# Performance work log

Hardware: AMD Instinct MI355X
Metric: run time of the kernel (lower is better)

## Reference

```python
import jax, jax.numpy as jnp
import numpy as np

H = 2048  # hidden_size
B, S = 4, 4096
LEVELS = 3  # hierarchical_compression_levels


def _linear_params(key, out_dim, in_dim):
    kw, kb = jax.random.split(key)
    bound = 1.0 / np.sqrt(in_dim)
    W = jax.random.uniform(kw, (out_dim, in_dim), minval=-bound, maxval=bound, dtype=jnp.float32)
    b = jax.random.uniform(kb, (out_dim,), minval=-bound, maxval=bound, dtype=jnp.float32)
    return W, b


def setup_inputs() -> dict:
    key = jax.random.key(0)
    ks = jax.random.split(key, 12)
    inp = {}
    inp['hidden_states'] = jax.random.normal(ks[0], (B, S, H), dtype=jnp.float32)
    inp['access_frequency'] = jax.random.uniform(ks[1], (B, S), dtype=jnp.float32)
    inp['importance_score'] = jax.random.uniform(ks[2], (B, S), dtype=jnp.float32)
    # compression level 1: H -> H/2 -> H/2 -> H ; level 2: H -> H/4 -> H/4 -> H
    inp['comp1_W'], inp['comp1_b'] = _linear_params(ks[3], H // 2, H)
    inp['adapt1_W'], inp['adapt1_b'] = _linear_params(ks[4], H // 2, H // 2)
    inp['decomp1_W'], inp['decomp1_b'] = _linear_params(ks[5], H, H // 2)
    inp['comp2_W'], inp['comp2_b'] = _linear_params(ks[6], H // 4, H)
    inp['adapt2_W'], inp['adapt2_b'] = _linear_params(ks[7], H // 4, H // 4)
    inp['decomp2_W'], inp['decomp2_b'] = _linear_params(ks[8], H, H // 4)
    # strategy selector: Linear(H, H/4) -> ReLU -> Linear(H/4, LEVELS) -> Softmax
    inp['sel1_W'], inp['sel1_b'] = _linear_params(ks[9], H // 4, H)
    inp['sel2_W'], inp['sel2_b'] = _linear_params(ks[10], LEVELS, H // 4)
    return inp


def reference(hidden_states, access_frequency, importance_score,
              comp1_W, comp1_b, adapt1_W, adapt1_b, decomp1_W, decomp1_b,
              comp2_W, comp2_b, adapt2_W, adapt2_b, decomp2_W, decomp2_b,
              sel1_W, sel1_b, sel2_W, sel2_b):
    h = hidden_states
    h2 = h.shape[-1] // 2
    # _get_compression_strategy: scale first half by freq, second half by importance
    combined = jnp.concatenate(
        [h[..., :h2] * access_frequency[..., None],
         h[..., h2:] * importance_score[..., None]], axis=-1)  # [B,S,H]
    hid = jax.nn.relu(jnp.einsum('bsh,oh->bso', combined, sel1_W) + sel1_b)
    strategy_weights = jax.nn.softmax(jnp.einsum('bso,lo->bsl', hid, sel2_W) + sel2_b, axis=-1)
    selected = jnp.argmax(strategy_weights, axis=-1)  # [B,S] int

    def branch(Wc, bc, Wa, ba, Wd, bd):
        c = jnp.einsum('bsh,oh->bso', h, Wc) + bc          # compress
        c = jnp.einsum('bso,po->bsp', c, Wa) + ba          # frequency adaptor
        return jnp.einsum('bsp,hp->bsh', c, Wd) + bd       # decompress

    out1 = branch(comp1_W, comp1_b, adapt1_W, adapt1_b, decomp1_W, decomp1_b)
    out2 = branch(comp2_W, comp2_b, adapt2_W, adapt2_b, decomp2_W, decomp2_b)
    stacked = jnp.stack([h, out1, out2], axis=2)  # [B,S,LEVELS,H]
    compressed = jnp.take_along_axis(stacked, selected[:, :, None, None], axis=2)[:, :, 0, :]
    return compressed
```

## Files before the change

### kernel.cpp

```cpp
#include <hip/hip_runtime.h>
#include <hip/hip_bf16.h>

#define TOK 16384
#define TAU2 0.001f

typedef __attribute__((ext_vector_type(8))) short short8;
typedef __attribute__((ext_vector_type(4))) float f32x4;

__device__ __forceinline__ unsigned short f32_bf16(float f) {
  __hip_bfloat16 h = __float2bfloat16(f);
  unsigned short u;
  __builtin_memcpy(&u, &h, sizeof(u));
  return u;
}
__device__ __forceinline__ float bf16_f32(unsigned short u) {
  union { unsigned int i; float f; } c; c.i = ((unsigned int)u) << 16; return c.f;
}

__global__ void zero_int(int* p) { if (threadIdx.x == 0) *p = 0; }

__global__ void cvt_kernel(const float* __restrict__ s, unsigned short* __restrict__ d, int n4) {
  int i = blockIdx.x * 256 + threadIdx.x;
  if (i < n4) {
    float4 v = ((const float4*)s)[i];
    union { unsigned short u[4]; uint2 q; } pk;
    pk.u[0] = f32_bf16(v.x); pk.u[1] = f32_bf16(v.y);
    pk.u[2] = f32_bf16(v.z); pk.u[3] = f32_bf16(v.w);
    ((uint2*)d)[i] = pk.q;
  }
}

__global__ void cvt_split_kernel(const float* __restrict__ s,
                                 unsigned short* __restrict__ dhi,
                                 unsigned short* __restrict__ dlo, int n4) {
  int i = blockIdx.x * 256 + threadIdx.x;
  if (i < n4) {
    float4 v = ((const float4*)s)[i];
    const float* f = (const float*)&v;
    union { unsigned short u[4]; uint2 q; } hi, lo;
    #pragma unroll
    for (int e = 0; e < 4; e++) {
      unsigned short h = f32_bf16(f[e]);
      hi.u[e] = h;
      lo.u[e] = f32_bf16(f[e] - bf16_f32(h));
    }
    ((uint2*)dhi)[i] = hi.q;
    ((uint2*)dlo)[i] = lo.q;
  }
}

template<int AMODE, int EPI>
__global__ __launch_bounds__(256, 2)
void gemm_tile(const void* __restrict__ Av,
               const unsigned short* __restrict__ Bw,
               const unsigned short* __restrict__ Bw2,
               const float* __restrict__ bias,
               void* __restrict__ Outv,
               const int* __restrict__ sel, int branch,
               const float* __restrict__ scA, const float* __restrict__ scB,
               int M, int N, int K) {
  __shared__ __align__(16) unsigned short As[(AMODE == 3 ? 2 : 1) * 128 * 32];
  __shared__ __align__(16) unsigned short Bs[(AMODE == 3 ? 2 : 1) * 128 * 32];
  const int LO = 128 * 32;
  const int tid = threadIdx.x;
  const int m0 = blockIdx.y * 128, n0 = blockIdx.x * 128;
  const int lane = tid & 63, wave = tid >> 6;
  const int wm = wave >> 1, wn = wave & 1;
  const int quad = lane >> 4, lr = lane & 15;
  const int srow = tid >> 1, scol = (tid & 1) * 16;

  f32x4 acc[4][4] = {};

  for (int k0 = 0; k0 < K; k0 += 32) {
    if (AMODE == 2) {
      const unsigned short* A = (const unsigned short*)Av;
      const uint4* src = (const uint4*)(A + (size_t)(m0 + srow) * K + k0 + scol);
      uint4* dst = (uint4*)(As + srow * 32 + scol);
      dst[0] = src[0]; dst[1] = src[1];
    } else {
      const float* A = (const float*)Av;
      const float4* src = (const float4*)(A + (size_t)(m0 + srow) * K + k0 + scol);
      float4 f[4];
      f[0] = src[0]; f[1] = src[1]; f[2] = src[2]; f[3] = src[3];
      float s = 1.0f;
      if (AMODE == 3) {
        int tk = m0 + srow;
        s = ((k0 + scol) * 2 < K) ? scA[tk] : scB[tk];
      }
      union { unsigned short u[16]; uint4 q[2]; } hi;
      union { unsigned short u[16]; uint4 q[2]; } lo;
      const float* ff = (const float*)f;
      #pragma unroll
      for (int e = 0; e < 16; e++) {
        float fv = ff[e];
        if (AMODE == 3) fv *= s;
        unsigned short hb = f32_bf16(fv);
        hi.u[e] = hb;
        if (AMODE == 3) lo.u[e] = f32_bf16(fv - bf16_f32(hb));
      }
      uint4* dst = (uint4*)(As + srow * 32 + scol);
      dst[0] = hi.q[0]; dst[1] = hi.q[1];
      if (AMODE == 3) {
        uint4* dst2 = (uint4*)(As + LO + srow * 32 + scol);
        dst2[0] = lo.q[0]; dst2[1] = lo.q[1];
      }
    }
    {
      const uint4* src = (const uint4*)(Bw + (size_t)(n0 + srow) * K + k0 + scol);
      uint4* dst = (uint4*)(Bs + srow * 32 + scol);
      dst[0] = src[0]; dst[1] = src[1];
      if (AMODE == 3) {
        const uint4* src2 = (const uint4*)(Bw2 + (size_t)(n0 + srow) * K + k0 + scol);
        uint4* dst2 = (uint4*)(Bs + LO + srow * 32 + scol);
        dst2[0] = src2[0]; dst2[1] = src2[1];
      }
    }
    __syncthreads();
    short8 af[4], bfr[4];
    #pragma unroll
    for (int i = 0; i < 4; i++)
      af[i] = *(const short8*)(As + (wm * 64 + i * 16 + lr) * 32 + quad * 8);
    #pragma unroll
    for (int j = 0; j < 4; j++)
      bfr[j] = *(const short8*)(Bs + (wn * 64 + j * 16 + lr) * 32 + quad * 8);
    if (AMODE == 3) {
      short8 af2[4], bf2[4];
      #pragma unroll
      for (int i = 0; i < 4; i++)
        af2[i] = *(const short8*)(As + LO + (wm * 64 + i * 16 + lr) * 32 + quad * 8);
      #pragma unroll
      for (int j = 0; j < 4; j++)
        bf2[j] = *(const short8*)(Bs + LO + (wn * 64 + j * 16 + lr) * 32 + quad * 8);
      #pragma unroll
      for (int i = 0; i < 4; i++)
        #pragma unroll
        for (int j = 0; j < 4; j++) {
          acc[i][j] = __builtin_amdgcn_mfma_f32_16x16x32_bf16(af[i], bfr[j], acc[i][j], 0, 0, 0);
          acc[i][j] = __builtin_amdgcn_mfma_f32_16x16x32_bf16(af[i], bf2[j], acc[i][j], 0, 0, 0);
          acc[i][j] = __builtin_amdgcn_mfma_f32_16x16x32_bf16(af2[i], bfr[j], acc[i][j], 0, 0, 0);
        }
    } else {
      #pragma unroll
      for (int i = 0; i < 4; i++)
        #pragma unroll
        for (int j = 0; j < 4; j++)
          acc[i][j] = __builtin_amdgcn_mfma_f32_16x16x32_bf16(af[i], bfr[j], acc[i][j], 0, 0, 0);
    }
    __syncthreads();
  }

  #pragma unroll
  for (int i = 0; i < 4; i++) {
    const int rbase = m0 + wm * 64 + i * 16 + quad * 4;
    #pragma unroll
    for (int j = 0; j < 4; j++) {
      const int col = n0 + wn * 64 + j * 16 + lr;
      const float bv = bias[col];
      #pragma unroll
      for (int r = 0; r < 4; r++) {
        const int row = rbase + r;
        float v = acc[i][j][r] + bv;
        if (EPI == 0) {
          ((unsigned short*)Outv)[(size_t)row * N + col] = f32_bf16(v);
        } else if (EPI == 1) {
          ((unsigned short*)Outv)[(size_t)row * N + col] = f32_bf16(fmaxf(v, 0.0f));
        } else if (EPI == 2) {
          if (sel[row] == branch) ((float*)Outv)[(size_t)row * N + col] = v;
        } else {
          ((float*)Outv)[(size_t)row * N + col] = fmaxf(v, 0.0f);
        }
      }
    }
  }
}

__global__ __launch_bounds__(256)
void selector_logits_f32(const float* __restrict__ hidf,
                         const float* __restrict__ W2, const float* __restrict__ b2,
                         int* __restrict__ sel, int* __restrict__ risky,
                         int* __restrict__ riskyCount) {
  const int wave = threadIdx.x >> 6, lane = threadIdx.x & 63;
  const int token = blockIdx.x * 4 + wave;
  const float* hs = hidf + (size_t)token * 512 + lane * 8;
  float4 h0 = *(const float4*)hs, h1 = *(const float4*)(hs + 4);
  float p[3];
  #pragma unroll
  for (int c = 0; c < 3; c++) {
    const float* w = W2 + c * 512 + lane * 8;
    float4 w0 = *(const float4*)w, w1 = *(const float4*)(w + 4);
    p[c] = h0.x*w0.x + h0.y*w0.y + h0.z*w0.z + h0.w*w0.w
         + h1.x*w1.x + h1.y*w1.y + h1.z*w1.z + h1.w*w1.w;
  }
  #pragma unroll
  for (int off = 32; off >= 1; off >>= 1) {
    #pragma unroll
    for (int c = 0; c < 3; c++) p[c] += __shfl_xor(p[c], off, 64);
  }
  if (lane == 0) {
    float l0 = p[0] + b2[0], l1 = p[1] + b2[1], l2 = p[2] + b2[2];
    int arg = 0; float best = l0;
    if (l1 > best) { best = l1; arg = 1; }
    if (l2 > best) { best = l2; arg = 2; }
    float second;
    if (arg == 0) second = fmaxf(l1, l2);
    else if (arg == 1) second = fmaxf(l0, l2);
    else second = fmaxf(l0, l1);
    sel[token] = arg;
    if (best - second < TAU2) {
      int idx = atomicAdd(riskyCount, 1);
      risky[idx] = token;
    }
  }
}

__global__ __launch_bounds__(256)
void recheck_exact(const float* __restrict__ h, const float* __restrict__ freq,
                   const float* __restrict__ imp,
                   const float* __restrict__ W1, const float* __restrict__ b1,
                   const float* __restrict__ W2, const float* __restrict__ b2,
                   const int* __restrict__ risky, const int* __restrict__ riskyCount,
                   int* __restrict__ sel) {
  __shared__ float h_sh[2048];
  __shared__ float hid_sh[512];
  const int n = *riskyCount;
  const int tid = threadIdx.x;
  for (int ri = blockIdx.x; ri < n; ri += gridDim.x) {
    const int token = risky[ri];
    {
      const float s = (tid < 128) ? freq[token] : imp[token];
      const float4* src = (const float4*)(h + (size_t)token * 2048) + tid * 2;
      float4 v0 = src[0], v1 = src[1];
      v0.x *= s; v0.y *= s; v0.z *= s; v0.w *= s;
      v1.x *= s; v1.y *= s; v1.z *= s; v1.w *= s;
      ((float4*)h_sh)[tid * 2] = v0;
      ((float4*)h_sh)[tid * 2 + 1] = v1;
    }
    __syncthreads();
    #pragma unroll
    for (int half = 0; half < 2; half++) {
      const int o = tid + half * 256;
      const float* wrow = W1 + (size_t)o * 2048;
      float a0 = 0.f, a1 = 0.f, a2 = 0.f, a3 = 0.f;
      for (int k = 0; k < 2048; k += 16) {
        float4 w0 = *(const float4*)(wrow + k);
        float4 w1v = *(const float4*)(wrow + k + 4);
        float4 w2v = *(const float4*)(wrow + k + 8);
        float4 w3v = *(const float4*)(wrow + k + 12);
        float4 x0 = *(const float4*)(h_sh + k);
        float4 x1 = *(const float4*)(h_sh + k + 4);
        float4 x2 = *(const float4*)(h_sh + k + 8);
        float4 x3 = *(const float4*)(h_sh + k + 12);
        a0 += w0.x*x0.x + w0.y*x0.y + w0.z*x0.z + w0.w*x0.w;
        a1 += w1v.x*x1.x + w1v.y*x1.y + w1v.z*x1.z + w1v.w*x1.w;
        a2 += w2v.x*x2.x + w2v.y*x2.y + w2v.z*x2.z + w2v.w*x2.w;
        a3 += w3v.x*x3.x + w3v.y*x3.y + w3v.z*x3.z + w3v.w*x3.w;
      }
      hid_sh[o] = fmaxf((a0 + a1) + (a2 + a3) + b1[o], 0.0f);
    }
    __syncthreads();
    if (tid < 64) {
      const int lane = tid;
      const float* hs = &hid_sh[lane * 8];
      float l[3];
      #pragma unroll
      for (int c = 0; c < 3; c++) {
        const float* w = W2 + c * 512 + lane * 8;
        float s = 0.0f;
        #pragma unroll
        for (int e = 0; e < 8; e++) s += hs[e] * w[e];
        l[c] = s;
      }
      #pragma unroll
      for (int off = 32; off >= 1; off >>= 1)
        #pragma unroll
        for (int c = 0; c < 3; c++) l[c] += __shfl_xor(l[c], off, 64);
      if (lane == 0) {
        float l0 = l[0] + b2[0], l1 = l[1] + b2[1], l2 = l[2] + b2[2];
        int arg = 0; float best = l0;
        if (l1 > best) { best = l1; arg = 1; }
        if (l2 > best) { arg = 2; }
        sel[token] = arg;
      }
    }
    __syncthreads();
  }
}

__global__ __launch_bounds__(256)
void copy_sel0(const float* __restrict__ h, const int* __restrict__ sel,
               float* __restrict__ out) {
  const int token = blockIdx.x;
  if (sel[token] != 0) return;
  const float4* src = (const float4*)(h + (size_t)token * 2048);
  float4* dst = (float4*)(out + (size_t)token * 2048);
  dst[threadIdx.x] = src[threadIdx.x];
  dst[threadIdx.x + 256] = src[threadIdx.x + 256];
}

extern "C" void kernel_launch(void* const* d_in, const int* in_sizes, int n_in,
                              void* d_out, int out_size, void* d_ws, size_t ws_size,
                              hipStream_t stream) {
  const float* h        = (const float*)d_in[0];
  const float* freq     = (const float*)d_in[1];
  const float* imp      = (const float*)d_in[2];
  const float* comp1W   = (const float*)d_in[3];
  const float* comp1b   = (const float*)d_in[4];
  const float* adapt1W  = (const float*)d_in[5];
  const float* adapt1b  = (const float*)d_in[6];
  const float* decomp1W = (const float*)d_in[7];
  const float* decomp1b = (const float*)d_in[8];
  const float* comp2W   = (const float*)d_in[9];
  const float* comp2b   = (const float*)d_in[10];
  const float* adapt2W  = (const float*)d_in[11];
  const float* adapt2b  = (const float*)d_in[12];
  const float* decomp2W = (const float*)d_in[13];
  const float* decomp2b = (const float*)d_in[14];
  const float* sel1W    = (const float*)d_in[15];
  const float* sel1b    = (const float*)d_in[16];
  const float* sel2W    = (const float*)d_in[17];
  const float* sel2b    = (const float*)d_in[18];
  float* out = (float*)d_out;

  char* ws = (char*)d_ws;
  size_t off = 0;
  auto alloc = [&](size_t bytes) -> void* {
    void* p = ws + off; off += (bytes + 255) & ~(size_t)255; return p;
  };
  unsigned short* wb_comp1   = (unsigned short*)alloc((size_t)1024 * 2048 * 2);
  unsigned short* wb_adapt1  = (unsigned short*)alloc((size_t)1024 * 1024 * 2);
  unsigned short* wb_decomp1 = (unsigned short*)alloc((size_t)2048 * 1024 * 2);
  unsigned short* wb_comp2   = (unsigned short*)alloc((size_t)512 * 2048 * 2);
  unsigned short* wb_adapt2  = (unsigned short*)alloc((size_t)512 * 512 * 2);
  unsigned short* wb_decomp2 = (unsigned short*)alloc((size_t)2048 * 512 * 2);
  unsigned short* w1hi       = (unsigned short*)alloc((size_t)512 * 2048 * 2);
  unsigned short* w1lo       = (unsigned short*)alloc((size_t)512 * 2048 * 2);
  float*          hidf       = (float*)alloc((size_t)TOK * 512 * 4);
  unsigned short* c1         = (unsigned short*)alloc((size_t)TOK * 1024 * 2);
  unsigned short* a1         = (unsigned short*)alloc((size_t)TOK * 1024 * 2);
  int* sel        = (int*)alloc((size_t)TOK * 4);
  int* risky      = (int*)alloc((size_t)TOK * 4);
  int* riskyCount = (int*)alloc(256);
  unsigned short* c2 = c1;
  unsigned short* a2 = a1;

  zero_int<<<1, 64, 0, stream>>>(riskyCount);

  auto cvt = [&](const float* s, unsigned short* d, int n) {
    cvt_kernel<<<(n / 4 + 255) / 256, 256, 0, stream>>>(s, d, n / 4);
  };
  cvt(comp1W,   wb_comp1,   1024 * 2048);
  cvt(adapt1W,  wb_adapt1,  1024 * 1024);
  cvt(decomp1W, wb_decomp1, 2048 * 1024);
  cvt(comp2W,   wb_comp2,   512 * 2048);
  cvt(adapt2W,  wb_adapt2,  512 * 512);
  cvt(decomp2W, wb_decomp2, 2048 * 512);
  cvt_split_kernel<<<(512 * 2048 / 4 + 255) / 256, 256, 0, stream>>>(
      sel1W, w1hi, w1lo, 512 * 2048 / 4);

  gemm_tile<3, 3><<<dim3(512 / 128, TOK / 128), 256, 0, stream>>>(
      h, w1hi, w1lo, sel1b, hidf, nullptr, 0, freq, imp, TOK, 512, 2048);
  selector_logits_f32<<<TOK / 4, 256, 0, stream>>>(hidf, sel2W, sel2b, sel, risky, riskyCount);
  recheck_exact<<<256, 256, 0, stream>>>(h, freq, imp, sel1W, sel1b, sel2W, sel2b,
                                         risky, riskyCount, sel);

  gemm_tile<0, 0><<<dim3(1024 / 128, TOK / 128), 256, 0, stream>>>(
      h, wb_comp1, nullptr, comp1b, c1, nullptr, 0, nullptr, nullptr, TOK, 1024, 2048);
  gemm_tile<2, 0><<<dim3(1024 / 128, TOK / 128), 256, 0, stream>>>(
      c1, wb_adapt1, nullptr, adapt1b, a1, nullptr, 0, nullptr, nullptr, TOK, 1024, 1024);
  gemm_tile<2, 2><<<dim3(2048 / 128, TOK / 128), 256, 0, stream>>>(
      a1, wb_decomp1, nullptr, decomp1b, out, sel, 1, nullptr, nullptr, TOK, 2048, 1024);

  gemm_tile<0, 0><<<dim3(512 / 128, TOK / 128), 256, 0, stream>>>(
      h, wb_comp2, nullptr, comp2b, c2, nullptr, 0, nullptr, nullptr, TOK, 512, 2048);
  gemm_tile<2, 0><<<dim3(512 / 128, TOK / 128), 256, 0, stream>>>(
      c2, wb_adapt2, nullptr, adapt2b, a2, nullptr, 0, nullptr, nullptr, TOK, 512, 512);
  gemm_tile<2, 2><<<dim3(2048 / 128, TOK / 128), 256, 0, stream>>>(
      a2, wb_decomp2, nullptr, decomp2b, out, sel, 2, nullptr, nullptr, TOK, 2048, 512);

  copy_sel0<<<TOK, 256, 0, stream>>>(h, sel, out);
}
```

Measured before the change: 1.060 ms.

## Compact tokens per selected branch and run branch GEMMs only on them

Builds per-branch token index lists from the selector output with atomics, pads each list to a multiple of 128, and has the branch GEMMs gather A rows through the index and scatter outputs back. Blocks beyond the padded count exit early, so each branch computes only for tokens that selected it instead of all tokens. This adds two small kernels and indirect row addressing, and produces a nondeterministic token order in the compacted buffers.

```diff
diff --git a/kernel.cpp b/kernel.cpp
--- a/kernel.cpp
+++ b/kernel.cpp
@@ -17,7 +17,9 @@
   union { unsigned int i; float f; } c; c.i = ((unsigned int)u) << 16; return c.f;
 }
 
-__global__ void zero_int(int* p) { if (threadIdx.x == 0) *p = 0; }
+__global__ void zero3(int* a, int* c) {
+  if (threadIdx.x == 0) { *a = 0; c[0] = 0; c[1] = 0; }
+}
 
 __global__ void cvt_kernel(const float* __restrict__ s, unsigned short* __restrict__ d, int n4) {
   int i = blockIdx.x * 256 + threadIdx.x;
@@ -49,37 +51,65 @@
   }
 }
 
-template<int AMODE, int EPI>
+__global__ void compact_sel(const int* __restrict__ sel, int* __restrict__ idx1,
+                            int* __restrict__ idx2, int* __restrict__ cnt) {
+  int t = blockIdx.x * 256 + threadIdx.x;
+  int s = sel[t];
+  if (s == 1) idx1[atomicAdd(&cnt[0], 1)] = t;
+  else if (s == 2) idx2[atomicAdd(&cnt[1], 1)] = t;
+}
+
+__global__ void pad_idx(int* __restrict__ idx1, int* __restrict__ idx2,
+                        const int* __restrict__ cnt, int* __restrict__ mc) {
+  const int tid = threadIdx.x;
+  const int n1 = cnt[0], n2 = cnt[1];
+  const int p1 = (n1 + 127) & ~(int)127, p2 = (n2 + 127) & ~(int)127;
+  if (tid < p1 - n1) idx1[n1 + tid] = -1;
+  if (tid < p2 - n2) idx2[n2 + tid] = -1;
+  if (tid == 0) { mc[0] = p1; mc[1] = p2; }
+}
+
+template<int AMODE, int EPI, int AG>
 __global__ __launch_bounds__(256, 2)
 void gemm_tile(const void* __restrict__ Av,
                const unsigned short* __restrict__ Bw,
                const unsigned short* __restrict__ Bw2,
                const float* __restrict__ bias,
                void* __restrict__ Outv,
-               const int* __restrict__ sel, int branch,
                const float* __restrict__ scA, const float* __restrict__ scB,
+               const int* __restrict__ idx, const int* __restrict__ mcp,
                int M, int N, int K) {
   __shared__ __align__(16) unsigned short As[(AMODE == 3 ? 2 : 1) * 128 * 32];
   __shared__ __align__(16) unsigned short Bs[(AMODE == 3 ? 2 : 1) * 128 * 32];
   const int LO = 128 * 32;
   const int tid = threadIdx.x;
   const int m0 = blockIdx.y * 128, n0 = blockIdx.x * 128;
+  if (mcp && m0 >= *mcp) return;
   const int lane = tid & 63, wave = tid >> 6;
   const int wm = wave >> 1, wn = wave & 1;
   const int quad = lane >> 4, lr = lane & 15;
   const int srow = tid >> 1, scol = (tid & 1) * 16;
 
+  size_t aRowOff;
+  {
+    int ar = m0 + srow;
+    if (AG) { int t = idx[ar]; ar = (t < 0) ? 0 : t; }
+    aRowOff = (size_t)ar * K;
+  }
+  const unsigned short* Brow = Bw + (size_t)(n0 + srow) * K;
+  const unsigned short* Brow2 = (AMODE == 3) ? (Bw2 + (size_t)(n0 + srow) * K) : nullptr;
+
   f32x4 acc[4][4] = {};
 
   for (int k0 = 0; k0 < K; k0 += 32) {
     if (AMODE == 2) {
       const unsigned short* A = (const unsigned short*)Av;
-      const uint4* src = (const uint4*)(A + (size_t)(m0 + srow) * K + k0 + scol);
+      const uint4* src = (const uint4*)(A + aRowOff + k0 + scol);
       uint4* dst = (uint4*)(As + srow * 32 + scol);
       dst[0] = src[0]; dst[1] = src[1];
     } else {
       const float* A = (const float*)Av;
-      const float4* src = (const float4*)(A + (size_t)(m0 + srow) * K + k0 + scol);
+      const float4* src = (const float4*)(A + aRowOff + k0 + scol);
       float4 f[4];
       f[0] = src[0]; f[1] = src[1]; f[2] = src[2]; f[3] = src[3];
       float s = 1.0f;
@@ -106,11 +136,11 @@
       }
     }
     {
-      const uint4* src = (const uint4*)(Bw + (size_t)(n0 + srow) * K + k0 + scol);
+      const uint4* src = (const uint4*)(Brow + k0 + scol);
       uint4* dst = (uint4*)(Bs + srow * 32 + scol);
       dst[0] = src[0]; dst[1] = src[1];
       if (AMODE == 3) {
-        const uint4* src2 = (const uint4*)(Bw2 + (size_t)(n0 + srow) * K + k0 + scol);
+        const uint4* src2 = (const uint4*)(Brow2 + k0 + scol);
         uint4* dst2 = (uint4*)(Bs + LO + srow * 32 + scol);
         dst2[0] = src2[0]; dst2[1] = src2[1];
       }
@@ -164,10 +194,11 @@
           ((unsigned short*)Outv)[(size_t)row * N + col] = f32_bf16(v);
         } else if (EPI == 1) {
           ((unsigned short*)Outv)[(size_t)row * N + col] = f32_bf16(fmaxf(v, 0.0f));
-        } else if (EPI == 2) {
-          if (sel[row] == branch) ((float*)Outv)[(size_t)row * N + col] = v;
+        } else if (EPI == 3) {
+          ((float*)Outv)[(size_t)row * N + col] = fmaxf(v, 0.0f);
         } else {
-          ((float*)Outv)[(size_t)row * N + col] = fmaxf(v, 0.0f);
+          const int t = idx[row];
+          if (t >= 0) ((float*)Outv)[(size_t)t * N + col] = v;
         }
       }
     }
@@ -340,10 +371,14 @@
   int* sel        = (int*)alloc((size_t)TOK * 4);
   int* risky      = (int*)alloc((size_t)TOK * 4);
   int* riskyCount = (int*)alloc(256);
+  int* idx1       = (int*)alloc((size_t)TOK * 4);
+  int* idx2       = (int*)alloc((size_t)TOK * 4);
+  int* cnt        = (int*)alloc(256);
+  int* mc         = (int*)alloc(256);
   unsigned short* c2 = c1;
   unsigned short* a2 = a1;
 
-  zero_int<<<1, 64, 0, stream>>>(riskyCount);
+  zero3<<<1, 64, 0, stream>>>(riskyCount, cnt);
 
   auto cvt = [&](const float* s, unsigned short* d, int n) {
     cvt_kernel<<<(n / 4 + 255) / 256, 256, 0, stream>>>(s, d, n / 4);
@@ -357,25 +392,28 @@
   cvt_split_kernel<<<(512 * 2048 / 4 + 255) / 256, 256, 0, stream>>>(
       sel1W, w1hi, w1lo, 512 * 2048 / 4);
 
-  gemm_tile<3, 3><<<dim3(512 / 128, TOK / 128), 256, 0, stream>>>(
-      h, w1hi, w1lo, sel1b, hidf, nullptr, 0, freq, imp, TOK, 512, 2048);
+  gemm_tile<3, 3, 0><<<dim3(512 / 128, TOK / 128), 256, 0, stream>>>(
+      h, w1hi, w1lo, sel1b, hidf, freq, imp, nullptr, nullptr, TOK, 512, 2048);
   selector_logits_f32<<<TOK / 4, 256, 0, stream>>>(hidf, sel2W, sel2b, sel, risky, riskyCount);
   recheck_exact<<<256, 256, 0, stream>>>(h, freq, imp, sel1W, sel1b, sel2W, sel2b,
                                          risky, riskyCount, sel);
 
-  gemm_tile<0, 0><<<dim3(1024 / 128, TOK / 128), 256, 0, stream>>>(
-      h, wb_comp1, nullptr, comp1b, c1, nullptr, 0, nullptr, nullptr, TOK, 1024, 2048);
-  gemm_tile<2, 0><<<dim3(1024 / 128, TOK / 128), 256, 0, stream>>>(
-      c1, wb_adapt1, nullptr, adapt1b, a1, nullptr, 0, nullptr, nullptr, TOK, 1024, 1024);
-  gemm_tile<2, 2><<<dim3(2048 / 128, TOK / 128), 256, 0, stream>>>(
-      a1, wb_decomp1, nullptr, decomp1b, out, sel, 1, nullptr, nullptr, TOK, 2048, 1024);
-
-  gemm_tile<0, 0><<<dim3(512 / 128, TOK / 128), 256, 0, stream>>>(
-      h, wb_comp2, nullptr, comp2b, c2, nullptr, 0, nullptr, nullptr, TOK, 512, 2048);
-  gemm_tile<2, 0><<<dim3(512 / 128, TOK / 128), 256, 0, stream>>>(
-      c2, wb_adapt2, nullptr, adapt2b, a2, nullptr, 0, nullptr, nullptr, TOK, 512, 512);
-  gemm_tile<2, 2><<<dim3(2048 / 128, TOK / 128), 256, 0, stream>>>(
-      a2, wb_decomp2, nullptr, decomp2b, out, sel, 2, nullptr, nullptr, TOK, 2048, 512);
+  compact_sel<<<TOK / 256, 256, 0, stream>>>(sel, idx1, idx2, cnt);
+  pad_idx<<<1, 256, 0, stream>>>(idx1, idx2, cnt, mc);
+
+  gemm_tile<0, 0, 1><<<dim3(1024 / 128, TOK / 128), 256, 0, stream>>>(
+      h, wb_comp1, nullptr, comp1b, c1, nullptr, nullptr, idx1, mc + 0, TOK, 1024, 2048);
+  gemm_tile<2, 0, 0><<<dim3(1024 / 128, TOK / 128), 256, 0, stream>>>(
+      c1, wb_adapt1, nullptr, adapt1b, a1, nullptr, nullptr, nullptr, mc + 0, TOK, 1024, 1024);
+  gemm_tile<2, 4, 0><<<dim3(2048 / 128, TOK / 128), 256, 0, stream>>>(
+      a1, wb_decomp1, nullptr, decomp1b, out, nullptr, nullptr, idx1, mc + 0, TOK, 2048, 1024);
+
+  gemm_tile<0, 0, 1><<<dim3(512 / 128, TOK / 128), 256, 0, stream>>>(
+      h, wb_comp2, nullptr, comp2b, c2, nullptr, nullptr, idx2, mc + 1, TOK, 512, 2048);
+  gemm_tile<2, 0, 0><<<dim3(512 / 128, TOK / 128), 256, 0, stream>>>(
+      c2, wb_adapt2, nullptr, adapt2b, a2, nullptr, nullptr, nullptr, mc + 1, TOK, 512, 512);
+  gemm_tile<2, 4, 0><<<dim3(2048 / 128, TOK / 128), 256, 0, stream>>>(
+      a2, wb_decomp2, nullptr, decomp2b, out, nullptr, nullptr, idx2, mc + 1, TOK, 2048, 512);
 
   copy_sel0<<<TOK, 256, 0, stream>>>(h, sel, out);
 }
```

After: 997.3 us. 5.9% less time.
